# Kernel optimization log

Hardware: AMD Instinct MI355X
Metric: run time of the kernel (lower is better)

The kernel has to match this reference:

```python
import jax, jax.numpy as jnp
import numpy as np

# Bruxism rule tables (class, min, max) x 3 conditions x 13 combinations
BRUX_COMBOS = np.array([
    [[500, 0.1, 0.8], [41, 0.05, 0.5], [0, 0.0, 1.0]],
    [[369, 0.1, 0.5], [500, 0.1, 0.5], [0, 0.0, 1.0]],
    [[412, 0.05, 0.4], [431, 0.05, 0.4], [470, 0.05, 0.4]],
    [[127, 0.1, 0.8], [67, 0.1, 0.7], [103, 0.1, 0.6]],
    [[399, 0.1, 0.9], [403, 0.1, 0.8], [412, 0.1, 0.7]],
    [[410, 0.1, 0.9], [411, 0.1, 0.8], [398, 0.1, 0.7]],
    [[412, 0.1, 0.8], [410, 0.1, 0.7], [398, 0.1, 0.6]],
    [[435, 0.1, 0.9], [438, 0.1, 0.8], [449, 0.1, 0.7]],
    [[374, 0.1, 0.9], [436, 0.1, 0.8], [435, 0.1, 0.7]],
    [[372, 0.1, 0.9], [434, 0.1, 0.8], [469, 0.1, 0.7]],
    [[500, 0.1, 0.8], [439, 0.1, 0.7], [50, 0.1, 0.6]],
    [[399, 0.1, 0.9], [403, 0.1, 0.8], [410, 0.1, 0.7]],
    [[410, 0.1, 0.9], [398, 0.1, 0.8], [435, 0.1, 0.7]]], dtype=np.float32)
BRUX_SCORES = np.array([2.94, 1.76, 1.76, 1.47, 0.29, 0.88, 0.01, 0.29, 0.29, 0.01, 0.29, 0.01, 0.01], dtype=np.float32)
NON_BRUX_CLASSES = np.array([38, 42, 0], dtype=np.int32)
COUGH_CLASS = 42
NUM_FRAMES = 42  # total_score_size


def _group_classify(judge, score, gsize, min_valid, required):
    # judge/score: [B, F] bool/float; sliding groups of gsize, per tf while_loop logic
    F = judge.shape[-1]
    R = F - gsize + 1  # group_range
    win = jnp.arange(R)[:, None] + jnp.arange(gsize)[None, :]  # [R, gsize]
    gj = judge[:, win]            # [B, R, gsize]
    gs = score[:, win]            # [B, R, gsize]
    tc = jnp.sum(gj, axis=-1)
    grp_j = tc >= min_valid                                   # group judgement
    grp_s = jnp.where(grp_j, jnp.sum(jnp.where(gj, gs, 0.0), axis=-1), 0.0)
    cnt = jnp.sum(grp_j, axis=-1)
    ok = cnt >= required
    masked = jnp.where(grp_j, grp_s, -jnp.inf)
    top_vals = jax.lax.top_k(masked, required)[0]             # [B, required]
    total = jnp.where(ok, jnp.sum(top_vals, axis=-1), 0.0)
    return ok, total


def _forward(score):
    # score: [B, 42, C]
    B, F, C = score.shape
    flat = score.reshape(B * F, C)

    # ---- Bruxism per-frame judgement ----
    cls = jnp.asarray(BRUX_COMBOS[:, :, 0].astype(np.int32))   # [13,3]
    lo = jnp.asarray(BRUX_COMBOS[:, :, 1])
    hi = jnp.asarray(BRUX_COMBOS[:, :, 2])
    vals = flat[:, cls]                                        # [N,13,3]
    combo_pass = jnp.all((vals >= lo) & (vals <= hi), axis=-1) # [N,13]
    any_match = jnp.any(combo_pass, axis=-1)
    first = jnp.argmax(combo_pass, axis=-1)                    # index-1 of first passing combo
    _, idx10 = jax.lax.top_k(flat, 10)                         # [N,10]
    has_nb = jnp.any(idx10[:, :, None] == jnp.asarray(NON_BRUX_CLASSES)[None, None, :], axis=(1, 2))
    bf_judge = any_match & jnp.logical_not(has_nb)
    brux_table = jnp.round(jnp.asarray(BRUX_SCORES) * 100.0) / 100.0
    bf_score = jnp.where(bf_judge, brux_table[first], 0.0)

    # ---- Cough per-frame judgement ----
    s42 = flat[:, COUGH_CLASS]
    c_pass = (s42 >= 0.1) & (s42 <= 1.0)
    in_top10 = jnp.any(idx10 == COUGH_CLASS, axis=-1)
    cf_judge = c_pass | in_top10
    cf_score = jnp.where(c_pass, jnp.round(1.5 * 100.0) / 100.0, jnp.where(in_top10, 1.0, 0.0))

    bf_judge = bf_judge.reshape(B, F)
    bf_score = bf_score.reshape(B, F)
    cf_judge = cf_judge.reshape(B, F)
    cf_score = cf_score.reshape(B, F)

    # ---- Grouped window classification ----
    brux_j, brux_s = _group_classify(bf_judge, bf_score, gsize=4, min_valid=2, required=2)
    cough_j, cough_s = _group_classify(cf_judge, cf_score, gsize=3, min_valid=2, required=2)
    return brux_j, brux_s, cough_j, cough_s


def setup_inputs() -> dict:
    key = jax.random.key(0)
    score = jax.random.uniform(key, (2048, 42, 521), dtype=jnp.float32)
    return {"score": score}


def reference(score):
    return _forward(score)
```

## Files before the change

kernel.cpp:

```cpp
#include <hip/hip_runtime.h>
#include <math.h>

#define NB 2048
#define NF 42
#define NC 521

__constant__ int   d_ccls[39] = {
    500, 41,  0,
    369, 500, 0,
    412, 431, 470,
    127, 67,  103,
    399, 403, 412,
    410, 411, 398,
    412, 410, 398,
    435, 438, 449,
    374, 436, 435,
    372, 434, 469,
    500, 439, 50,
    399, 403, 410,
    410, 398, 435};
__constant__ float d_clo[39] = {
    0.1f, 0.05f, 0.0f,
    0.1f, 0.1f,  0.0f,
    0.05f,0.05f, 0.05f,
    0.1f, 0.1f,  0.1f,
    0.1f, 0.1f,  0.1f,
    0.1f, 0.1f,  0.1f,
    0.1f, 0.1f,  0.1f,
    0.1f, 0.1f,  0.1f,
    0.1f, 0.1f,  0.1f,
    0.1f, 0.1f,  0.1f,
    0.1f, 0.1f,  0.1f,
    0.1f, 0.1f,  0.1f,
    0.1f, 0.1f,  0.1f};
__constant__ float d_chi[39] = {
    0.8f, 0.5f, 1.0f,
    0.5f, 0.5f, 1.0f,
    0.4f, 0.4f, 0.4f,
    0.8f, 0.7f, 0.6f,
    0.9f, 0.8f, 0.7f,
    0.9f, 0.8f, 0.7f,
    0.8f, 0.7f, 0.6f,
    0.9f, 0.8f, 0.7f,
    0.9f, 0.8f, 0.7f,
    0.9f, 0.8f, 0.7f,
    0.8f, 0.7f, 0.6f,
    0.9f, 0.8f, 0.7f,
    0.9f, 0.8f, 0.7f};
__constant__ float d_btab[13] = {2.94f, 1.76f, 1.76f, 1.47f, 0.29f, 0.88f, 0.01f,
                                 0.29f, 0.29f, 0.01f, 0.29f, 0.01f, 0.01f};

__global__ __launch_bounds__(256, 8)
void sleep_cls_kernel(const float* __restrict__ score, float* __restrict__ out) {
    const int b    = blockIdx.x;
    const int tid  = threadIdx.x;
    const int wave = tid >> 6;
    const int lane = tid & 63;
    const float* base = score + (size_t)b * (NF * NC);

    __shared__ int   s_bfj[NF];
    __shared__ float s_bfs[NF];
    __shared__ int   s_cfj[NF];
    __shared__ float s_cfs[NF];

    for (int f = wave; f < NF; f += 4) {
        const float* row = base + f * NC;
        const float v0  = row[0];
        const float v38 = row[38];
        const float v42 = row[42];

        float vv[8];
#pragma unroll
        for (int k = 0; k < 8; ++k) vv[k] = row[lane + (k << 6)];

        int cnt = 0;
        {
            const float v = vv[0];
            const int   j = lane;
            cnt += (int)(v > v0)
                 + ((int)((v > v38) || ((v == v38) && (j < 38))) << 10)
                 + ((int)((v > v42) || ((v == v42) && (j < 42))) << 20);
        }
#pragma unroll
        for (int k = 1; k < 8; ++k) {
            const float v = vv[k];
            cnt += (int)(v > v0) + ((int)(v > v38) << 10) + ((int)(v > v42) << 20);
        }
        if (lane < 9) {
            const float v = row[lane + 512];
            cnt += (int)(v > v0) + ((int)(v > v38) << 10) + ((int)(v > v42) << 20);
        }
#pragma unroll
        for (int s = 32; s > 0; s >>= 1) cnt += __shfl_xor(cnt, s);

        const int  c0  = cnt & 1023;
        const int  c38 = (cnt >> 10) & 1023;
        const int  c42 = (cnt >> 20) & 1023;
        const bool in0  = c0  < 10;
        const bool in38 = c38 < 10;
        const bool in42 = c42 < 10;
        const bool has_nb = in0 || in38 || in42;

        bool pass = false;
        if (lane < 13) {
            const int base3 = lane * 3;
            const float a0 = row[d_ccls[base3 + 0]];
            const float a1 = row[d_ccls[base3 + 1]];
            const float a2 = row[d_ccls[base3 + 2]];
            pass = (a0 >= d_clo[base3 + 0]) & (a0 <= d_chi[base3 + 0]) &
                   (a1 >= d_clo[base3 + 1]) & (a1 <= d_chi[base3 + 1]) &
                   (a2 >= d_clo[base3 + 2]) & (a2 <= d_chi[base3 + 2]);
        }
        const unsigned long long cm = __ballot(pass);
        const bool any   = (cm != 0ull);
        const int  first = any ? __builtin_ctzll(cm) : 0;

        const bool  bfj = any && !has_nb;
        const float bfs = bfj ? d_btab[first] : 0.0f;

        const bool  cpass = (v42 >= 0.1f) && (v42 <= 1.0f);
        const bool  cfj   = cpass || in42;
        const float cfs   = cpass ? 1.5f : (in42 ? 1.0f : 0.0f);

        if (lane == 0) {
            s_bfj[f] = (int)bfj;
            s_bfs[f] = bfs;
            s_cfj[f] = (int)cfj;
            s_cfs[f] = cfs;
        }
    }
    __syncthreads();

    if (wave < 2) {
        const int R = (wave == 0) ? 39 : 40;
        const int G = (wave == 0) ? 4 : 3;
        const int*   jarr = (wave == 0) ? s_bfj : s_cfj;
        const float* sarr = (wave == 0) ? s_bfs : s_cfs;

        bool  gj = false;
        float gs = -INFINITY;
        if (lane < R) {
            int   tc = 0;
            float ss = 0.0f;
            for (int k = 0; k < G; ++k) {
                tc += jarr[lane + k];
                ss += sarr[lane + k];
            }
            gj = (tc >= 2);
            gs = gj ? ss : -INFINITY;
        }
        const unsigned long long jm = __ballot(gj);
        const bool ok = __popcll(jm) >= 2;

        float m1 = gs;
#pragma unroll
        for (int s = 32; s > 0; s >>= 1) m1 = fmaxf(m1, __shfl_xor(m1, s));
        const unsigned long long em = __ballot(gs == m1);
        const int amax = __builtin_ctzll(em);
        float gs2 = (lane == amax) ? -INFINITY : gs;
        float m2 = gs2;
#pragma unroll
        for (int s = 32; s > 0; s >>= 1) m2 = fmaxf(m2, __shfl_xor(m2, s));

        if (lane == 0) {
            const int jo = (wave == 0) ? 0 : 2 * NB;
            const int so = (wave == 0) ? NB : 3 * NB;
            out[jo + b] = ok ? 1.0f : 0.0f;
            out[so + b] = ok ? (m1 + m2) : 0.0f;
        }
    }
}

extern "C" void kernel_launch(void* const* d_in, const int* in_sizes, int n_in,
                              void* d_out, int out_size, void* d_ws, size_t ws_size,
                              hipStream_t stream) {
    const float* score = (const float*)d_in[0];
    float* out = (float*)d_out;
    sleep_cls_kernel<<<dim3(NB), dim3(256), 0, stream>>>(score, out);
}
```

Baseline: 249.3 us.

## Split into per-frame kernel and per-batch grouping kernel via workspace

Replaces the single per-batch kernel, which looped each wave over about 11 frames, with a frame kernel where each wave handles exactly one row. Per-frame results go to a float4 workspace, and a second kernel does the sliding-window grouping with shuffles, one wave per batch element. This exposes more independent waves and issues all loads up front, including the class lookups and tail, to raise memory-level parallelism. The cost is an extra kernel launch, a global workspace round trip, and slightly redundant loads.

Result: faster. 238.5 us (-4.3%).

```diff
diff --git a/kernel.cpp b/kernel.cpp
--- a/kernel.cpp
+++ b/kernel.cpp
@@ -4,6 +4,7 @@
 #define NB 2048
 #define NF 42
 #define NC 521
+#define NROWS (NB * NF)
 
 __constant__ int   d_ccls[39] = {
     500, 41,  0,
@@ -51,122 +52,125 @@
                                  0.29f, 0.29f, 0.01f, 0.29f, 0.01f, 0.01f};
 
 __global__ __launch_bounds__(256, 8)
-void sleep_cls_kernel(const float* __restrict__ score, float* __restrict__ out) {
-    const int b    = blockIdx.x;
-    const int tid  = threadIdx.x;
-    const int wave = tid >> 6;
-    const int lane = tid & 63;
-    const float* base = score + (size_t)b * (NF * NC);
+void frame_kernel(const float* __restrict__ score, float4* __restrict__ ws) {
+    const int wave = threadIdx.x >> 6;
+    const int lane = threadIdx.x & 63;
+    const int gid  = blockIdx.x * 4 + wave;
+    const float* row = score + (size_t)gid * NC;
 
-    __shared__ int   s_bfj[NF];
-    __shared__ float s_bfs[NF];
-    __shared__ int   s_cfj[NF];
-    __shared__ float s_cfs[NF];
+    float vv[8];
+#pragma unroll
+    for (int k = 0; k < 8; ++k) vv[k] = row[lane + (k << 6)];
+    const float tail = row[512 + (lane < 9 ? lane : 8)];
+    const int c3 = (lane < 13 ? lane : 0) * 3;
+    const float a0 = row[d_ccls[c3 + 0]];
+    const float a1 = row[d_ccls[c3 + 1]];
+    const float a2 = row[d_ccls[c3 + 2]];
 
-    for (int f = wave; f < NF; f += 4) {
-        const float* row = base + f * NC;
-        const float v0  = row[0];
-        const float v38 = row[38];
-        const float v42 = row[42];
+    const float v0  = __shfl(vv[0], 0);
+    const float v38 = __shfl(vv[0], 38);
+    const float v42 = __shfl(vv[0], 42);
+    const float tl  = (lane < 9) ? tail : 0.0f;
 
-        float vv[8];
+    int cnt;
+    {
+        const float v = vv[0];
+        cnt = (int)(v > v0)
+            + ((int)((v > v38) || ((v == v38) && (lane < 38))) << 10)
+            + ((int)((v > v42) || ((v == v42) && (lane < 42))) << 20);
+    }
 #pragma unroll
-        for (int k = 0; k < 8; ++k) vv[k] = row[lane + (k << 6)];
+    for (int k = 1; k < 8; ++k) {
+        const float v = vv[k];
+        cnt += (int)(v > v0) + ((int)(v > v38) << 10) + ((int)(v > v42) << 20);
+    }
+    cnt += (int)(tl > v0) + ((int)(tl > v38) << 10) + ((int)(tl > v42) << 20);
+#pragma unroll
+    for (int s = 32; s > 0; s >>= 1) cnt += __shfl_xor(cnt, s);
 
-        int cnt = 0;
-        {
-            const float v = vv[0];
-            const int   j = lane;
-            cnt += (int)(v > v0)
-                 + ((int)((v > v38) || ((v == v38) && (j < 38))) << 10)
-                 + ((int)((v > v42) || ((v == v42) && (j < 42))) << 20);
-        }
-#pragma unroll
-        for (int k = 1; k < 8; ++k) {
-            const float v = vv[k];
-            cnt += (int)(v > v0) + ((int)(v > v38) << 10) + ((int)(v > v42) << 20);
-        }
-        if (lane < 9) {
-            const float v = row[lane + 512];
-            cnt += (int)(v > v0) + ((int)(v > v38) << 10) + ((int)(v > v42) << 20);
-        }
-#pragma unroll
-        for (int s = 32; s > 0; s >>= 1) cnt += __shfl_xor(cnt, s);
+    const bool in0  = (cnt & 1023) < 10;
+    const bool in38 = ((cnt >> 10) & 1023) < 10;
+    const bool in42 = ((cnt >> 20) & 1023) < 10;
+    const bool has_nb = in0 || in38 || in42;
 
-        const int  c0  = cnt & 1023;
-        const int  c38 = (cnt >> 10) & 1023;
-        const int  c42 = (cnt >> 20) & 1023;
-        const bool in0  = c0  < 10;
-        const bool in38 = c38 < 10;
-        const bool in42 = c42 < 10;
-        const bool has_nb = in0 || in38 || in42;
+    bool pass = false;
+    if (lane < 13) {
+        pass = (a0 >= d_clo[c3 + 0]) & (a0 <= d_chi[c3 + 0]) &
+               (a1 >= d_clo[c3 + 1]) & (a1 <= d_chi[c3 + 1]) &
+               (a2 >= d_clo[c3 + 2]) & (a2 <= d_chi[c3 + 2]);
+    }
+    const unsigned long long cm = __ballot(pass);
+    const bool any   = (cm != 0ull);
+    const int  first = any ? __builtin_ctzll(cm) : 0;
 
-        bool pass = false;
-        if (lane < 13) {
-            const int base3 = lane * 3;
-            const float a0 = row[d_ccls[base3 + 0]];
-            const float a1 = row[d_ccls[base3 + 1]];
-            const float a2 = row[d_ccls[base3 + 2]];
-            pass = (a0 >= d_clo[base3 + 0]) & (a0 <= d_chi[base3 + 0]) &
-                   (a1 >= d_clo[base3 + 1]) & (a1 <= d_chi[base3 + 1]) &
-                   (a2 >= d_clo[base3 + 2]) & (a2 <= d_chi[base3 + 2]);
-        }
-        const unsigned long long cm = __ballot(pass);
-        const bool any   = (cm != 0ull);
-        const int  first = any ? __builtin_ctzll(cm) : 0;
+    const bool  bfj = any && !has_nb;
+    const float bfs = bfj ? d_btab[first] : 0.0f;
 
-        const bool  bfj = any && !has_nb;
-        const float bfs = bfj ? d_btab[first] : 0.0f;
+    const bool  cpass = (v42 >= 0.1f) && (v42 <= 1.0f);
+    const bool  cfj   = cpass || in42;
+    const float cfs   = cpass ? 1.5f : (in42 ? 1.0f : 0.0f);
 
-        const bool  cpass = (v42 >= 0.1f) && (v42 <= 1.0f);
-        const bool  cfj   = cpass || in42;
-        const float cfs   = cpass ? 1.5f : (in42 ? 1.0f : 0.0f);
+    if (lane == 0)
+        ws[gid] = make_float4(bfj ? 1.0f : 0.0f, bfs, cfj ? 1.0f : 0.0f, cfs);
+}
 
-        if (lane == 0) {
-            s_bfj[f] = (int)bfj;
-            s_bfs[f] = bfs;
-            s_cfj[f] = (int)cfj;
-            s_cfs[f] = cfs;
-        }
-    }
-    __syncthreads();
+__global__ __launch_bounds__(256)
+void group_kernel(const float4* __restrict__ ws, float* __restrict__ out) {
+    const int wave = threadIdx.x >> 6;
+    const int lane = threadIdx.x & 63;
+    const int b    = blockIdx.x * 4 + wave;
 
-    if (wave < 2) {
-        const int R = (wave == 0) ? 39 : 40;
-        const int G = (wave == 0) ? 4 : 3;
-        const int*   jarr = (wave == 0) ? s_bfj : s_cfj;
-        const float* sarr = (wave == 0) ? s_bfs : s_cfs;
+    float4 v = make_float4(0.0f, 0.0f, 0.0f, 0.0f);
+    if (lane < NF) v = ws[b * NF + lane];
+    const float bfj = v.x, bfs = v.y, cfj = v.z, cfs = v.w;
 
-        bool  gj = false;
-        float gs = -INFINITY;
-        if (lane < R) {
-            int   tc = 0;
-            float ss = 0.0f;
-            for (int k = 0; k < G; ++k) {
-                tc += jarr[lane + k];
-                ss += sarr[lane + k];
-            }
-            gj = (tc >= 2);
-            gs = gj ? ss : -INFINITY;
-        }
+    {
+        const float j1 = __shfl_down(bfj, 1), j2 = __shfl_down(bfj, 2), j3 = __shfl_down(bfj, 3);
+        const float s1 = __shfl_down(bfs, 1), s2 = __shfl_down(bfs, 2), s3 = __shfl_down(bfs, 3);
+        const float tc = ((bfj + j1) + j2) + j3;
+        const float ss = ((bfs + s1) + s2) + s3;
+        const bool  gj = (lane < 39) && (tc >= 2.0f);
+        float gs = gj ? ss : -INFINITY;
+
         const unsigned long long jm = __ballot(gj);
         const bool ok = __popcll(jm) >= 2;
-
         float m1 = gs;
 #pragma unroll
         for (int s = 32; s > 0; s >>= 1) m1 = fmaxf(m1, __shfl_xor(m1, s));
         const unsigned long long em = __ballot(gs == m1);
         const int amax = __builtin_ctzll(em);
-        float gs2 = (lane == amax) ? -INFINITY : gs;
-        float m2 = gs2;
+        float m2 = (lane == amax) ? -INFINITY : gs;
 #pragma unroll
         for (int s = 32; s > 0; s >>= 1) m2 = fmaxf(m2, __shfl_xor(m2, s));
 
         if (lane == 0) {
-            const int jo = (wave == 0) ? 0 : 2 * NB;
-            const int so = (wave == 0) ? NB : 3 * NB;
-            out[jo + b] = ok ? 1.0f : 0.0f;
-            out[so + b] = ok ? (m1 + m2) : 0.0f;
+            out[b]      = ok ? 1.0f : 0.0f;
+            out[NB + b] = ok ? (m1 + m2) : 0.0f;
+        }
+    }
+
+    {
+        const float j1 = __shfl_down(cfj, 1), j2 = __shfl_down(cfj, 2);
+        const float s1 = __shfl_down(cfs, 1), s2 = __shfl_down(cfs, 2);
+        const float tc = (cfj + j1) + j2;
+        const float ss = (cfs + s1) + s2;
+        const bool  gj = (lane < 40) && (tc >= 2.0f);
+        float gs = gj ? ss : -INFINITY;
+
+        const unsigned long long jm = __ballot(gj);
+        const bool ok = __popcll(jm) >= 2;
+        float m1 = gs;
+#pragma unroll
+        for (int s = 32; s > 0; s >>= 1) m1 = fmaxf(m1, __shfl_xor(m1, s));
+        const unsigned long long em = __ballot(gs == m1);
+        const int amax = __builtin_ctzll(em);
+        float m2 = (lane == amax) ? -INFINITY : gs;
+#pragma unroll
+        for (int s = 32; s > 0; s >>= 1) m2 = fmaxf(m2, __shfl_xor(m2, s));
+
+        if (lane == 0) {
+            out[2 * NB + b] = ok ? 1.0f : 0.0f;
+            out[3 * NB + b] = ok ? (m1 + m2) : 0.0f;
         }
     }
 }
@@ -176,5 +180,7 @@
                               hipStream_t stream) {
     const float* score = (const float*)d_in[0];
     float* out = (float*)d_out;
-    sleep_cls_kernel<<<dim3(NB), dim3(256), 0, stream>>>(score, out);
+    float4* ws = (float4*)d_ws;
+    frame_kernel<<<dim3(NROWS / 4), dim3(256), 0, stream>>>(score, ws);
+    group_kernel<<<dim3(NB / 4), dim3(256), 0, stream>>>(ws, out);
 }
```
